# Optimization experiments

Measured on AMD Instinct MI355X. Metric: run time of the kernel, lower is better.

## Reference

```python
import jax, jax.numpy as jnp
import numpy as np

IN_F = 2048
OUT_F = 2048
G = 5 + 3  # grid_size + spline_order
BATCH = 8192


def setup_inputs() -> dict:
    key = jax.random.key(0)
    k1, k2, k3 = jax.random.split(key, 3)
    x = jax.random.normal(k1, (BATCH, IN_F), dtype=jnp.float32)
    # kaiming_uniform(a=sqrt(5)) on (out,in): bound = 1/sqrt(in)
    bound = 1.0 / np.sqrt(IN_F)
    base_weight = jax.random.uniform(k2, (OUT_F, IN_F), dtype=jnp.float32,
                                     minval=-bound, maxval=bound)
    grid = 0.1 * jax.random.normal(k3, (IN_F, OUT_F, G), dtype=jnp.float32)
    return {"x": x, "base_weight": base_weight, "grid": grid}


def reference(x, base_weight, grid):
    # base branch: standard linear  (B, out)
    base_out = x @ base_weight.T
    # spline branch: Gaussian basis around the scalar grid mean  (B, in)
    basis = jnp.exp(-jnp.square(x - grid.mean()))
    # contract over in_features and the grid dim: sum_i sum_g basis[b,i]*grid[i,o,g]
    spline_out = basis @ grid.sum(axis=-1)  # (B, out)
    return base_out + spline_out
```

## Files before the change

### kernel.cpp

```cpp
#include <hip/hip_runtime.h>

#define IN_F   2048
#define OUT_F  2048
#define GDIM   8
#define BATCH  8192
#define KDIM   4096
#define GRID_TOTAL_INV (1.0f / 33554432.0f)

#define BK     64
#define NKT    (KDIM / BK)
#define BUFSZ  65536
#define BOFF   32768
#define REG    16384

typedef __bf16 bf16x8 __attribute__((ext_vector_type(8)));
typedef float  f32x4  __attribute__((ext_vector_type(4)));
typedef unsigned short u16x8 __attribute__((ext_vector_type(8)));

__device__ __forceinline__ unsigned short f2bf(float f) {
  union { float f; unsigned int u; } v; v.f = f;
  unsigned int r = v.u + 0x7fffu + ((v.u >> 16) & 1u);
  return (unsigned short)(r >> 16);
}

__device__ __forceinline__ void gload_lds16(const void* g, void* l) {
  __builtin_amdgcn_global_load_lds(
      (const __attribute__((address_space(1))) void*)g,
      (__attribute__((address_space(3))) void*)l, 16, 0, 0);
}

__global__ __launch_bounds__(256) void prep_bw(const float* __restrict__ bw,
                                               unsigned short* __restrict__ Bt,
                                               float* __restrict__ sum_ptr) {
  if (blockIdx.x == 0 && threadIdx.x == 0) *sum_ptr = 0.0f;
  size_t i8 = ((size_t)blockIdx.x * 256 + threadIdx.x) * 8;
  const float4* p = reinterpret_cast<const float4*>(bw + i8);
  float4 a = p[0], b = p[1];
  u16x8 v;
  v[0] = f2bf(a.x); v[1] = f2bf(a.y); v[2] = f2bf(a.z); v[3] = f2bf(a.w);
  v[4] = f2bf(b.x); v[5] = f2bf(b.y); v[6] = f2bf(b.z); v[7] = f2bf(b.w);
  size_t o = i8 >> 11;
  size_t k = i8 & 2047;
  *reinterpret_cast<u16x8*>(Bt + o * KDIM + k) = v;
}

__global__ __launch_bounds__(256) void prep_grid(const float* __restrict__ grid,
                                                 unsigned short* __restrict__ Bt,
                                                 float* __restrict__ sum_ptr) {
  __shared__ float tile[32][33];
  __shared__ float wsum[4];
  int bi = blockIdx.x >> 6;
  int bo = blockIdx.x & 63;
  int i0 = bi << 5, o0 = bo << 5;
  int t = threadIdx.x;
  float local = 0.f;
#pragma unroll
  for (int p = 0; p < 4; ++p) {
    int li = t + 256 * p;
    int il = li >> 5, ol = li & 31;
    const float4* g4 = reinterpret_cast<const float4*>(
        grid + ((size_t)(i0 + il) * OUT_F + (size_t)(o0 + ol)) * GDIM);
    float4 a = g4[0], b = g4[1];
    float s = ((a.x + a.y) + (a.z + a.w)) + ((b.x + b.y) + (b.z + b.w));
    tile[il][ol] = s;
    local += s;
  }
#pragma unroll
  for (int off = 32; off >= 1; off >>= 1) local += __shfl_down(local, off, 64);
  int lane = t & 63, w = t >> 6;
  if (lane == 0) wsum[w] = local;
  __syncthreads();
#pragma unroll
  for (int p = 0; p < 4; ++p) {
    int li = t + 256 * p;
    int ol = li >> 5, il = li & 31;
    Bt[(size_t)(o0 + ol) * KDIM + IN_F + (i0 + il)] = f2bf(tile[il][ol]);
  }
  if (t == 0) atomicAdd(sum_ptr, (wsum[0] + wsum[1]) + (wsum[2] + wsum[3]));
}

__global__ __launch_bounds__(256) void prep_A(const float* __restrict__ x,
                                              const float* __restrict__ sum_ptr,
                                              unsigned short* __restrict__ Abuf) {
  float m = *sum_ptr * GRID_TOTAL_INV;
  size_t i8 = ((size_t)blockIdx.x * 256 + threadIdx.x) * 8;
  const float4* p = reinterpret_cast<const float4*>(x + i8);
  float4 a = p[0], b = p[1];
  float xs[8] = {a.x, a.y, a.z, a.w, b.x, b.y, b.z, b.w};
  u16x8 xv, bv;
#pragma unroll
  for (int j = 0; j < 8; ++j) {
    xv[j] = f2bf(xs[j]);
    float d = xs[j] - m;
    bv[j] = f2bf(__expf(-d * d));
  }
  size_t bi = i8 >> 11;
  size_t k  = i8 & 2047;
  *reinterpret_cast<u16x8*>(Abuf + bi * KDIM + k) = xv;
  *reinterpret_cast<u16x8*>(Abuf + bi * KDIM + IN_F + k) = bv;
}

__global__ __launch_bounds__(512, 2) void gemm_kernel(
    const unsigned short* __restrict__ A,
    const unsigned short* __restrict__ B,
    float* __restrict__ C) {
  __shared__ __align__(16) char lds[2 * BUFSZ];
  const int t    = threadIdx.x;
  const int lane = t & 63;
  const int wid  = t >> 6;
  const int wm   = wid >> 2;
  const int wn   = wid & 3;
  const int bx = blockIdx.x;
  const int bm = ((bx & 7) << 2) | ((bx >> 3) & 3);
  const int bn = bx >> 5;

  f32x4 acc[8][4] = {};
  bf16x8 af[4], bf[4];

  const int cs = (t & 3) ^ ((t >> 4) & 3);
  const unsigned short* aStage = A + ((size_t)(bm * 256 + (t >> 2)) * KDIM) + cs * 8;
  const unsigned short* bStage = B + ((size_t)(bn * 256 + (t >> 2)) * KDIM) + cs * 8;
  const int dOff = t * 16;

  const int sc  = (lane >> 4) ^ ((lane >> 2) & 3);
  const int aRd = (wm * 128 + (lane & 15)) * 64 + sc * 16;
  const int bRd = (wn * 64  + (lane & 15)) * 64 + sc * 16;

#define STAGE_R(wb, kt, opOff, kk, src)                                        \
  gload_lds16((src) + (size_t)(kt) * BK + (kk) * 32,                           \
              (wb) + (opOff) + (kk) * REG + dOff);                             \
  gload_lds16((src) + 128 * KDIM + (size_t)(kt) * BK + (kk) * 32,              \
              (wb) + (opOff) + (kk) * REG + 8192 + dOff);

#define DSREAD_A(rb, kk, mb)                                                   \
  _Pragma("unroll")                                                            \
  for (int i_ = 0; i_ < 4; ++i_)                                               \
    af[i_] = *reinterpret_cast<const bf16x8*>(                                 \
        (rb) + (kk) * REG + aRd + ((mb) + i_) * 1024);

#define DSREAD_B(rb, kk)                                                       \
  _Pragma("unroll")                                                            \
  for (int n_ = 0; n_ < 4; ++n_)                                               \
    bf[n_] = *reinterpret_cast<const bf16x8*>(                                 \
        (rb) + BOFF + (kk) * REG + bRd + n_ * 1024);

#define LGKM0                                                                  \
  asm volatile("s_waitcnt lgkmcnt(0)" ::: "memory");                           \
  __builtin_amdgcn_sched_barrier(0);

#define MFMAQ(mb)                                                              \
  __builtin_amdgcn_s_setprio(1);                                               \
  _Pragma("unroll")                                                            \
  for (int i_ = 0; i_ < 4; ++i_)                                               \
    _Pragma("unroll")                                                          \
    for (int n_ = 0; n_ < 4; ++n_)                                             \
      acc[(mb) + i_][n_] = __builtin_amdgcn_mfma_f32_16x16x32_bf16(            \
          af[i_], bf[n_], acc[(mb) + i_][n_], 0, 0, 0);                        \
  __builtin_amdgcn_s_setprio(0);

#define VMCNT(n) asm volatile("s_waitcnt vmcnt(" #n ")" ::: "memory");

  STAGE_R(lds, 0, 0,    0, aStage);
  STAGE_R(lds, 0, BOFF, 0, bStage);
  STAGE_R(lds, 0, 0,    1, aStage);
  STAGE_R(lds, 0, BOFF, 1, bStage);

  for (int kt = 0; kt < NKT - 1; ++kt) {
    const char* rb = lds + (kt & 1) * BUFSZ;
    char* wb = lds + ((kt + 1) & 1) * BUFSZ;
    STAGE_R(wb, kt + 1, 0, 0, aStage);
    VMCNT(6);
    __builtin_amdgcn_s_barrier();
    DSREAD_A(rb, 0, 0); DSREAD_B(rb, 0);
    LGKM0; MFMAQ(0);
    DSREAD_A(rb, 0, 4);
    STAGE_R(wb, kt + 1, BOFF, 0, bStage);
    LGKM0; MFMAQ(4);
    STAGE_R(wb, kt + 1, 0, 1, aStage);
    VMCNT(6);
    __builtin_amdgcn_s_barrier();
    DSREAD_A(rb, 1, 0); DSREAD_B(rb, 1);
    LGKM0; MFMAQ(0);
    DSREAD_A(rb, 1, 4);
    STAGE_R(wb, kt + 1, BOFF, 1, bStage);
    LGKM0; MFMAQ(4);
  }
  {
    const char* rb = lds + ((NKT - 1) & 1) * BUFSZ;
    VMCNT(4);
    __builtin_amdgcn_s_barrier();
    DSREAD_A(rb, 0, 0); DSREAD_B(rb, 0); LGKM0; MFMAQ(0);
    DSREAD_A(rb, 0, 4);                  LGKM0; MFMAQ(4);
    VMCNT(0);
    __builtin_amdgcn_s_barrier();
    DSREAD_A(rb, 1, 0); DSREAD_B(rb, 1); LGKM0; MFMAQ(0);
    DSREAD_A(rb, 1, 4);                  LGKM0; MFMAQ(4);
  }

  const int rg = lane >> 4, cc = lane & 15;
  const size_t crow0 = (size_t)bm * 256 + wm * 128;
  const size_t ccol0 = (size_t)bn * 256 + wn * 64;
#pragma unroll
  for (int m = 0; m < 8; ++m)
#pragma unroll
    for (int n = 0; n < 4; ++n)
#pragma unroll
      for (int rr = 0; rr < 4; ++rr) {
        size_t row = crow0 + (size_t)m * 16 + rg * 4 + rr;
        size_t col = ccol0 + (size_t)n * 16 + cc;
        C[row * OUT_F + col] = acc[m][n][rr];
      }
}

extern "C" void kernel_launch(void* const* d_in, const int* in_sizes, int n_in,
                              void* d_out, int out_size, void* d_ws, size_t ws_size,
                              hipStream_t stream) {
  const float* x    = (const float*)d_in[0];
  const float* bw   = (const float*)d_in[1];
  const float* grid = (const float*)d_in[2];
  float* out = (float*)d_out;

  unsigned short* Abuf = (unsigned short*)d_ws;
  unsigned short* Bt   = Abuf + (size_t)BATCH * KDIM;
  float* sum_ptr = (float*)(Bt + (size_t)OUT_F * KDIM);

  prep_bw  <<<(OUT_F * IN_F / 8) / 256, 256, 0, stream>>>(bw, Bt, sum_ptr);
  prep_grid<<<64 * 64,                  256, 0, stream>>>(grid, Bt, sum_ptr);
  prep_A   <<<(BATCH * IN_F / 8) / 256, 256, 0, stream>>>(x, sum_ptr, Abuf);
  gemm_kernel<<<256, 512, 0, stream>>>(Abuf, Bt, out);
}
```

Measured before the change: 398.2 us.

## Restructure GEMM main loop into barrier-phased ping-pong fragment schedule

Splits A/B fragment registers into two sets and reorders the K-loop so LDS reads for each quarter are issued before the global-to-LDS staging, with extra workgroup barriers bracketing every MFMA block in a phased ping-pong style. The goal is to keep waves in lockstep so LDS reads, global loads and MFMA bursts interleave across the two co-resident waves per SIMD. It adds many more s_barrier calls and more live fragment registers, which could raise register pressure at the 512x2 launch bounds. Barrier placement relative to vmcnt waits changes, which risks correctness races on the LDS buffers.

```diff
diff --git a/kernel.cpp b/kernel.cpp
--- a/kernel.cpp
+++ b/kernel.cpp
@@ -115,7 +115,7 @@
   const int bn = bx >> 5;
 
   f32x4 acc[8][4] = {};
-  bf16x8 af[4], bf[4];
+  bf16x8 afA[4], afB[4], bfA[4], bfB[4];
 
   const int cs = (t & 3) ^ ((t >> 4) & 3);
   const unsigned short* aStage = A + ((size_t)(bm * 256 + (t >> 2)) * KDIM) + cs * 8;
@@ -132,69 +132,79 @@
   gload_lds16((src) + 128 * KDIM + (size_t)(kt) * BK + (kk) * 32,              \
               (wb) + (opOff) + (kk) * REG + 8192 + dOff);
 
-#define DSREAD_A(rb, kk, mb)                                                   \
+#define PH_READ_A(dst, rb, kk, mb)                                             \
   _Pragma("unroll")                                                            \
   for (int i_ = 0; i_ < 4; ++i_)                                               \
-    af[i_] = *reinterpret_cast<const bf16x8*>(                                 \
+    dst[i_] = *reinterpret_cast<const bf16x8*>(                                \
         (rb) + (kk) * REG + aRd + ((mb) + i_) * 1024);
 
-#define DSREAD_B(rb, kk)                                                       \
+#define PH_READ_B(dst, rb, kk)                                                 \
   _Pragma("unroll")                                                            \
   for (int n_ = 0; n_ < 4; ++n_)                                               \
-    bf[n_] = *reinterpret_cast<const bf16x8*>(                                 \
+    dst[n_] = *reinterpret_cast<const bf16x8*>(                                \
         (rb) + BOFF + (kk) * REG + bRd + n_ * 1024);
+
+#define SBAR0 __builtin_amdgcn_sched_barrier(0);
 
 #define LGKM0                                                                  \
   asm volatile("s_waitcnt lgkmcnt(0)" ::: "memory");                           \
   __builtin_amdgcn_sched_barrier(0);
 
-#define MFMAQ(mb)                                                              \
+#define MFMA16(a_, b_, mb)                                                     \
   __builtin_amdgcn_s_setprio(1);                                               \
   _Pragma("unroll")                                                            \
   for (int i_ = 0; i_ < 4; ++i_)                                               \
     _Pragma("unroll")                                                          \
     for (int n_ = 0; n_ < 4; ++n_)                                             \
       acc[(mb) + i_][n_] = __builtin_amdgcn_mfma_f32_16x16x32_bf16(            \
-          af[i_], bf[n_], acc[(mb) + i_][n_], 0, 0, 0);                        \
+          a_[i_], b_[n_], acc[(mb) + i_][n_], 0, 0, 0);                        \
   __builtin_amdgcn_s_setprio(0);
 
 #define VMCNT(n) asm volatile("s_waitcnt vmcnt(" #n ")" ::: "memory");
+
+#define BAR __builtin_amdgcn_s_barrier();
 
   STAGE_R(lds, 0, 0,    0, aStage);
   STAGE_R(lds, 0, BOFF, 0, bStage);
   STAGE_R(lds, 0, 0,    1, aStage);
   STAGE_R(lds, 0, BOFF, 1, bStage);
+  VMCNT(4);
+  BAR;
 
   for (int kt = 0; kt < NKT - 1; ++kt) {
     const char* rb = lds + (kt & 1) * BUFSZ;
     char* wb = lds + ((kt + 1) & 1) * BUFSZ;
+    PH_READ_A(afA, rb, 0, 0); PH_READ_B(bfA, rb, 0);
     STAGE_R(wb, kt + 1, 0, 0, aStage);
-    VMCNT(6);
-    __builtin_amdgcn_s_barrier();
-    DSREAD_A(rb, 0, 0); DSREAD_B(rb, 0);
-    LGKM0; MFMAQ(0);
-    DSREAD_A(rb, 0, 4);
+    SBAR0; BAR;
+    LGKM0; MFMA16(afA, bfA, 0);
+    BAR;
+    PH_READ_A(afB, rb, 0, 4);
     STAGE_R(wb, kt + 1, BOFF, 0, bStage);
-    LGKM0; MFMAQ(4);
+    VMCNT(4); SBAR0; BAR;
+    LGKM0; MFMA16(afB, bfA, 4);
+    BAR;
+    PH_READ_A(afA, rb, 1, 0); PH_READ_B(bfB, rb, 1);
     STAGE_R(wb, kt + 1, 0, 1, aStage);
-    VMCNT(6);
-    __builtin_amdgcn_s_barrier();
-    DSREAD_A(rb, 1, 0); DSREAD_B(rb, 1);
-    LGKM0; MFMAQ(0);
-    DSREAD_A(rb, 1, 4);
+    SBAR0; BAR;
+    LGKM0; MFMA16(afA, bfB, 0);
+    BAR;
+    PH_READ_A(afB, rb, 1, 4);
     STAGE_R(wb, kt + 1, BOFF, 1, bStage);
-    LGKM0; MFMAQ(4);
+    VMCNT(4); SBAR0; BAR;
+    LGKM0; MFMA16(afB, bfB, 4);
+    BAR;
   }
   {
     const char* rb = lds + ((NKT - 1) & 1) * BUFSZ;
-    VMCNT(4);
-    __builtin_amdgcn_s_barrier();
-    DSREAD_A(rb, 0, 0); DSREAD_B(rb, 0); LGKM0; MFMAQ(0);
-    DSREAD_A(rb, 0, 4);                  LGKM0; MFMAQ(4);
-    VMCNT(0);
-    __builtin_amdgcn_s_barrier();
-    DSREAD_A(rb, 1, 0); DSREAD_B(rb, 1); LGKM0; MFMAQ(0);
-    DSREAD_A(rb, 1, 4);                  LGKM0; MFMAQ(4);
+    PH_READ_A(afA, rb, 0, 0); PH_READ_B(bfA, rb, 0);
+    SBAR0; BAR; LGKM0; MFMA16(afA, bfA, 0); BAR;
+    PH_READ_A(afB, rb, 0, 4);
+    VMCNT(0); SBAR0; BAR; LGKM0; MFMA16(afB, bfA, 4); BAR;
+    PH_READ_A(afA, rb, 1, 0); PH_READ_B(bfB, rb, 1);
+    SBAR0; BAR; LGKM0; MFMA16(afA, bfB, 0); BAR;
+    PH_READ_A(afB, rb, 1, 4);
+    LGKM0; MFMA16(afB, bfB, 4);
   }
 
   const int rg = lane >> 4, cc = lane & 15;
```

After: 402.2 us. Within noise of the previous version (+1.0%).
